# Kernel tuning notes

Measured on AMD Instinct MI355X. Metric: run time of the kernel, lower is better.

The kernel has to match this reference:

```python
import jax, jax.numpy as jnp
import numpy as np

B, S, D, H = 2, 2048, 1024, 16
HD = D // H  # head_dim = 64

def setup_inputs() -> dict:
    key = jax.random.key(0)
    ks = jax.random.split(key, 5)
    scale = 1.0 / np.sqrt(D)
    x = jax.random.normal(ks[0], (B, S, D), dtype=jnp.float32)
    Wq = jax.random.normal(ks[1], (D, D), dtype=jnp.float32) * scale
    Wk = jax.random.normal(ks[2], (D, D), dtype=jnp.float32) * scale
    Wv = jax.random.normal(ks[3], (D, D), dtype=jnp.float32) * scale
    Wf = jax.random.normal(ks[4], (D, D), dtype=jnp.float32) * scale
    z = jnp.zeros((D,), dtype=jnp.float32)
    return {"x": x, "Wq": Wq, "bq": z, "Wk": Wk, "bk": z, "Wv": Wv, "bv": z, "Wf": Wf, "bf": z}

def reference(x, Wq, bq, Wk, bk, Wv, bv, Wf, bf):
    # Linear layers follow torch convention: y = x @ W.T + b
    def split_heads(t):  # [B,S,D] -> [B,H,S,HD]
        return t.reshape(B, S, H, HD).transpose(0, 2, 1, 3)
    q = split_heads(x @ Wq.T + bq)
    k = split_heads(x @ Wk.T + bk)
    v = split_heads(x @ Wv.T + bv)
    scores = jnp.einsum('bhqd,bhkd->bhqk', q, k) / jnp.sqrt(jnp.float32(HD))
    causal = jnp.tril(jnp.ones((S, S), dtype=bool))  # [S,S]
    scores = jnp.where(causal[None, None], scores, -jnp.inf)
    attn = jax.nn.softmax(scores, axis=-1)
    out = jnp.einsum('bhqk,bhkd->bhqd', attn, v)
    out = out.transpose(0, 2, 1, 3).reshape(B, S, D)
    return out @ Wf.T + bf
```

## Files before the change

### kernel.cpp

```cpp
#include <hip/hip_runtime.h>
#include <stdint.h>

#define B_  2
#define S_  2048
#define D_  1024
#define H_  16
#define HD_ 64
#define M_  (B_*S_)

typedef __bf16 bf16x8 __attribute__((ext_vector_type(8)));
typedef float  f32x4  __attribute__((ext_vector_type(4)));
typedef unsigned short u16x8 __attribute__((ext_vector_type(8)));

typedef const __attribute__((address_space(1))) void* gas_ptr;
typedef __attribute__((address_space(3))) void* las_ptr;

__device__ __forceinline__ uint16_t f32_to_bf16(float f) {
  uint32_t u = __float_as_uint(f);
  u += 0x7FFFu + ((u >> 16) & 1u);
  return (uint16_t)(u >> 16);
}

__device__ __forceinline__ uint16_t f32_to_bf16_rtz(float f) {
  return (uint16_t)(__float_as_uint(f) >> 16);
}

__device__ __forceinline__ void g2l16(const uint16_t* g, uint16_t* l) {
  __builtin_amdgcn_global_load_lds((gas_ptr)g, (las_ptr)l, 16, 0, 0);
}

#define POFF(rt, kt, h) ((size_t)((((rt) * 16 + (kt)) * 2 + (h)) * 4096))

__global__ void cast_pack(const float* __restrict__ x,
                          const float* __restrict__ wq, const float* __restrict__ wk,
                          const float* __restrict__ wv, const float* __restrict__ wf,
                          uint16_t* __restrict__ xb,
                          uint16_t* __restrict__ wqb, uint16_t* __restrict__ wkb,
                          uint16_t* __restrict__ wvb, uint16_t* __restrict__ wfb) {
  const int XC = M_ * D_ / 8;
  const int WC = D_ * D_ / 8;
  int i = blockIdx.x * 256 + threadIdx.x;
  const float* src; uint16_t* dst; int off;
  if (i < XC) { src = x; dst = xb; off = i; }
  else {
    int j = i - XC;
    int w = j >> 17;
    off = j & (WC - 1);
    src = (w == 0) ? wq : (w == 1) ? wk : (w == 2) ? wv : wf;
    dst = (w == 0) ? wqb : (w == 1) ? wkb : (w == 2) ? wvb : wfb;
  }
  const int row = off >> 7;
  const int c   = off & 127;
  const float4 v0 = ((const float4*)src)[row * 256 + c * 2];
  const float4 v1 = ((const float4*)src)[row * 256 + c * 2 + 1];
  u16x8 o;
  o[0] = f32_to_bf16(v0.x); o[1] = f32_to_bf16(v0.y);
  o[2] = f32_to_bf16(v0.z); o[3] = f32_to_bf16(v0.w);
  o[4] = f32_to_bf16(v1.x); o[5] = f32_to_bf16(v1.y);
  o[6] = f32_to_bf16(v1.z); o[7] = f32_to_bf16(v1.w);
  const int kt = c >> 3, c8 = c & 7, h = c8 >> 2, c4 = c8 & 3;
  const int rt = row >> 7, r = row & 127;
  const int s = 4 * r + (c4 ^ ((r >> 1) & 3));
  *(u16x8*)(dst + POFF(rt, kt, h) + s * 8) = o;
}

__global__ __launch_bounds__(256, 2)
void qkv_gemm(const uint16_t* __restrict__ xb,
              const uint16_t* __restrict__ wqb, const uint16_t* __restrict__ wkb,
              const uint16_t* __restrict__ wvb,
              const float* __restrict__ bqv, const float* __restrict__ bkv,
              const float* __restrict__ bvv,
              uint16_t* __restrict__ qout, uint16_t* __restrict__ kout,
              uint16_t* __restrict__ vtout)
{
  __shared__ __align__(16) uint16_t As[2][2][4096];
  __shared__ __align__(16) uint16_t Bs[2][2][4096];

  const int wsel = blockIdx.x >> 3;
  const int nsel = blockIdx.x & 7;
  const int mtile = blockIdx.y;
  const int tid  = threadIdx.x;
  const int lane = tid & 63, wave = tid >> 6;
  const int quad = lane >> 4, l16 = lane & 15;
  const int wm = (wave >> 1) * 64, wn = (wave & 1) * 64;
  const int sw = quad ^ ((l16 >> 1) & 3);

  const uint16_t *Ap, *Bp;
  int art, brt, m0e, n0e;
  if (wsel < 2) {
    Ap = xb; art = mtile; Bp = (wsel == 0) ? wqb : wkb; brt = nsel;
    m0e = mtile * 128; n0e = nsel * 128;
  } else {
    Ap = wvb; art = nsel; Bp = xb; brt = mtile;
    m0e = nsel * 128; n0e = mtile * 128;
  }

  const int se0 = tid * 8;
  const int se1 = (256 + tid) * 8;
  const int ld0 = (wave * 64) * 8;
  const int ld1 = (256 + wave * 64) * 8;

  f32x4 acc[4][4];
  #pragma unroll
  for (int i = 0; i < 4; ++i)
    #pragma unroll
    for (int j = 0; j < 4; ++j)
      #pragma unroll
      for (int e = 0; e < 4; ++e)
        acc[i][j][e] = 0.f;

  #pragma unroll
  for (int h = 0; h < 2; ++h) {
    g2l16(Ap + POFF(art, 0, h) + se0, &As[0][h][ld0]);
    g2l16(Ap + POFF(art, 0, h) + se1, &As[0][h][ld1]);
    g2l16(Bp + POFF(brt, 0, h) + se0, &Bs[0][h][ld0]);
    g2l16(Bp + POFF(brt, 0, h) + se1, &Bs[0][h][ld1]);
  }
  __syncthreads();

  for (int t = 0; t < 16; ++t) {
    const int cb = t & 1, cn = cb ^ 1;
    if (t < 15) {
      #pragma unroll
      for (int h = 0; h < 2; ++h) {
        g2l16(Ap + POFF(art, t + 1, h) + se0, &As[cn][h][ld0]);
        g2l16(Ap + POFF(art, t + 1, h) + se1, &As[cn][h][ld1]);
        g2l16(Bp + POFF(brt, t + 1, h) + se0, &Bs[cn][h][ld0]);
        g2l16(Bp + POFF(brt, t + 1, h) + se1, &Bs[cn][h][ld1]);
      }
    }
    bf16x8 af[4][2], bf[4][2];
    #pragma unroll
    for (int mt = 0; mt < 4; ++mt) {
      const int ro = ((wm + mt * 16 + l16) * 4 + sw) * 8;
      af[mt][0] = *(const bf16x8*)(&As[cb][0][ro]);
      af[mt][1] = *(const bf16x8*)(&As[cb][1][ro]);
    }
    #pragma unroll
    for (int nt = 0; nt < 4; ++nt) {
      const int ro = ((wn + nt * 16 + l16) * 4 + sw) * 8;
      bf[nt][0] = *(const bf16x8*)(&Bs[cb][0][ro]);
      bf[nt][1] = *(const bf16x8*)(&Bs[cb][1][ro]);
    }
    __builtin_amdgcn_s_setprio(1);
    #pragma unroll
    for (int mt = 0; mt < 4; ++mt)
      #pragma unroll
      for (int nt = 0; nt < 4; ++nt) {
        acc[mt][nt] = __builtin_amdgcn_mfma_f32_16x16x32_bf16(
            af[mt][0], bf[nt][0], acc[mt][nt], 0, 0, 0);
        acc[mt][nt] = __builtin_amdgcn_mfma_f32_16x16x32_bf16(
            af[mt][1], bf[nt][1], acc[mt][nt], 0, 0, 0);
      }
    __builtin_amdgcn_s_setprio(0);
    __syncthreads();
  }

  if (wsel < 2) {
    const float* bias = (wsel == 0) ? bqv : bkv;
    uint16_t* outp = (wsel == 0) ? qout : kout;
    const float scl = (wsel == 0) ? 0.18033688f : 1.0f;
    #pragma unroll
    for (int nt = 0; nt < 4; ++nt) {
      const int n = n0e + wn + nt * 16 + l16;
      const int h = n >> 6, hd = n & 63;
      const float bia = bias[n];
      #pragma unroll
      for (int mt = 0; mt < 4; ++mt) {
        #pragma unroll
        for (int r = 0; r < 4; ++r) {
          const int m = m0e + wm + mt * 16 + quad * 4 + r;
          const int bb = m >> 11, s = m & (S_ - 1);
          outp[(((size_t)(bb * H_ + h)) * S_ + s) * HD_ + hd] =
              f32_to_bf16((acc[mt][nt][r] + bia) * scl);
        }
      }
    }
  } else {
    #pragma unroll
    for (int mt = 0; mt < 4; ++mt) {
      #pragma unroll
      for (int r = 0; r < 4; ++r) {
        const int m = m0e + wm + mt * 16 + quad * 4 + r;
        const int h = m >> 6, hd = m & 63;
        const float bia = bvv[m];
        #pragma unroll
        for (int nt = 0; nt < 4; ++nt) {
          const int n = n0e + wn + nt * 16 + l16;
          const int bb = n >> 11, s = n & (S_ - 1);
          vtout[(((size_t)(bb * H_ + h)) * HD_ + hd) * S_ + s] =
              f32_to_bf16(acc[mt][nt][r] + bia);
        }
      }
    }
  }
}

__global__ __launch_bounds__(256)
void flash_attn(const uint16_t* __restrict__ qb, const uint16_t* __restrict__ kb,
                const uint16_t* __restrict__ vtb, uint16_t* __restrict__ ao)
{
  __shared__ __align__(16) uint16_t ks[2][2][2048];
  __shared__ __align__(16) uint16_t vs[2][2][2048];
  __shared__ __align__(16) uint16_t p_lds[4][16][72];

  const int bh = blockIdx.x;
  const int qt = (int)(gridDim.y - 1u - blockIdx.y);
  const int wave = threadIdx.x >> 6, lane = threadIdx.x & 63;
  const int quad = lane >> 4, l16 = lane & 15;
  const int sw = quad ^ ((l16 >> 1) & 3);
  const int q0 = qt * 64;

  const uint16_t* Q  = qb  + (size_t)bh * S_ * HD_;
  const uint16_t* Kp = kb  + (size_t)bh * S_ * HD_;
  const uint16_t* Vt = vtb + (size_t)bh * HD_ * S_;

  const int qrow = q0 + wave * 16;
  bf16x8 aq0 = *(const bf16x8*)(Q + (size_t)(qrow + l16) * HD_ + quad * 8);
  bf16x8 aq1 = *(const bf16x8*)(Q + (size_t)(qrow + l16) * HD_ + 32 + quad * 8);

  const int srow = lane >> 2;
  const int schk = (lane & 3) ^ ((lane >> 3) & 3);
  const uint16_t* sb[4]; uint16_t* sd0[4]; uint16_t* sd1[4]; int sstep[4];
  #pragma unroll
  for (int j = 0; j < 4; ++j) {
    const int g = wave * 4 + j;
    if (g < 8) {
      const int c = (g >> 2) & 1, rb = g & 3;
      sd0[j] = &ks[0][c][rb * 512];
      sd1[j] = &ks[1][c][rb * 512];
      sb[j] = Kp + (size_t)(rb * 16 + srow) * HD_ + c * 32 + schk * 8;
      sstep[j] = 64 * HD_;
    } else {
      const int gg = g - 8, c = (gg >> 2) & 1, rb = gg & 3;
      sd0[j] = &vs[0][c][rb * 512];
      sd1[j] = &vs[1][c][rb * 512];
      sb[j] = Vt + (size_t)(rb * 16 + srow) * S_ + c * 32 + schk * 8;
      sstep[j] = 64;
    }
  }

  float lpart[4];
  f32x4 o[4];
  #pragma unroll
  for (int r = 0; r < 4; ++r) lpart[r] = 0.f;
  #pragma unroll
  for (int t = 0; t < 4; ++t)
    #pragma unroll
    for (int e = 0; e < 4; ++e) o[t][e] = 0.f;

  const int rowid = qrow + quad * 4;

  #pragma unroll
  for (int j = 0; j < 4; ++j) {
    g2l16(sb[j], sd0[j]);
    sb[j] += sstep[j];
  }
  __syncthreads();

  for (int kt = 0; kt <= qt; ++kt) {
    const int kbase = kt * 64;
    const bool diag = (kt == qt);
    const int cb = kt & 1;

    if (kt < qt) {
      #pragma unroll
      for (int j = 0; j < 4; ++j) {
        g2l16(sb[j], cb ? sd0[j] : sd1[j]);
        sb[j] += sstep[j];
      }
    }

    bf16x8 kf0[4], kf1[4];
    #pragma unroll
    for (int nt = 0; nt < 4; ++nt) {
      kf0[nt] = *(const bf16x8*)(&ks[cb][0][((nt * 16 + l16) * 4 + sw) * 8]);
      kf1[nt] = *(const bf16x8*)(&ks[cb][1][((nt * 16 + l16) * 4 + sw) * 8]);
    }
    f32x4 sacc[4];
    __builtin_amdgcn_s_setprio(1);
    #pragma unroll
    for (int nt = 0; nt < 4; ++nt) {
      #pragma unroll
      for (int e = 0; e < 4; ++e) sacc[nt][e] = 0.f;
      sacc[nt] = __builtin_amdgcn_mfma_f32_16x16x32_bf16(aq0, kf0[nt], sacc[nt], 0, 0, 0);
      sacc[nt] = __builtin_amdgcn_mfma_f32_16x16x32_bf16(aq1, kf1[nt], sacc[nt], 0, 0, 0);
    }
    __builtin_amdgcn_s_setprio(0);

    bf16x8 vf0[4], vf1[4];
    #pragma unroll
    for (int t = 0; t < 4; ++t) {
      vf0[t] = *(const bf16x8*)(&vs[cb][0][((t * 16 + l16) * 4 + sw) * 8]);
      vf1[t] = *(const bf16x8*)(&vs[cb][1][((t * 16 + l16) * 4 + sw) * 8]);
    }

    #pragma unroll
    for (int nt = 0; nt < 4; ++nt) {
      const int kkc = kbase + nt * 16 + l16;
      #pragma unroll
      for (int r = 0; r < 4; ++r) {
        float p = __builtin_amdgcn_exp2f(sacc[nt][r]);
        if (diag && (kkc > rowid + r)) p = 0.f;
        lpart[r] += p;
        p_lds[wave][quad * 4 + r][nt * 16 + l16] = f32_to_bf16_rtz(p);
      }
    }

    bf16x8 ap0 = *(const bf16x8*)(&p_lds[wave][l16][quad * 8]);
    bf16x8 ap1 = *(const bf16x8*)(&p_lds[wave][l16][32 + quad * 8]);
    __builtin_amdgcn_s_setprio(1);
    #pragma unroll
    for (int t = 0; t < 4; ++t) {
      o[t] = __builtin_amdgcn_mfma_f32_16x16x32_bf16(ap0, vf0[t], o[t], 0, 0, 0);
      o[t] = __builtin_amdgcn_mfma_f32_16x16x32_bf16(ap1, vf1[t], o[t], 0, 0, 0);
    }
    __builtin_amdgcn_s_setprio(0);
    __syncthreads();
  }

  #pragma unroll
  for (int r = 0; r < 4; ++r) {
    lpart[r] += __shfl_xor(lpart[r], 1, 64);
    lpart[r] += __shfl_xor(lpart[r], 2, 64);
    lpart[r] += __shfl_xor(lpart[r], 4, 64);
    lpart[r] += __shfl_xor(lpart[r], 8, 64);
  }
  const int bb = bh >> 4, h = bh & 15;
  #pragma unroll
  for (int t = 0; t < 4; ++t) {
    const int c8 = t * 2 + (l16 >> 3);
    const int hh = c8 >> 2, c4 = c8 & 3, e = l16 & 7;
    #pragma unroll
    for (int r = 0; r < 4; ++r) {
      const float ov = o[t][r] / lpart[r];
      const int grow = bb * S_ + rowid + r;
      const int rt = grow >> 7, rr = grow & 127;
      const int s = 4 * rr + (c4 ^ ((rr >> 1) & 3));
      ao[POFF(rt, h, hh) + s * 8 + e] = f32_to_bf16(ov);
    }
  }
}

__global__ __launch_bounds__(256, 2)
void out_gemm(const uint16_t* __restrict__ ab, const uint16_t* __restrict__ wfb,
              const float* __restrict__ bfv, float* __restrict__ out)
{
  __shared__ __align__(16) uint16_t As[2][2][4096];
  __shared__ __align__(16) uint16_t Bs[2][2][4096];
  const int nsel = blockIdx.x;
  const int mtile = blockIdx.y;
  const int tid  = threadIdx.x;
  const int lane = tid & 63, wave = tid >> 6;
  const int quad = lane >> 4, l16 = lane & 15;
  const int wm = (wave >> 1) * 64, wn = (wave & 1) * 64;
  const int sw = quad ^ ((l16 >> 1) & 3);

  const int se0 = tid * 8, se1 = (256 + tid) * 8;
  const int ld0 = (wave * 64) * 8, ld1 = (256 + wave * 64) * 8;

  f32x4 acc[4][4];
  #pragma unroll
  for (int i = 0; i < 4; ++i)
    #pragma unroll
    for (int j = 0; j < 4; ++j)
      #pragma unroll
      for (int e = 0; e < 4; ++e)
        acc[i][j][e] = 0.f;

  #pragma unroll
  for (int h = 0; h < 2; ++h) {
    g2l16(ab  + POFF(mtile, 0, h) + se0, &As[0][h][ld0]);
    g2l16(ab  + POFF(mtile, 0, h) + se1, &As[0][h][ld1]);
    g2l16(wfb + POFF(nsel, 0, h) + se0, &Bs[0][h][ld0]);
    g2l16(wfb + POFF(nsel, 0, h) + se1, &Bs[0][h][ld1]);
  }
  __syncthreads();

  for (int t = 0; t < 16; ++t) {
    const int cb = t & 1, cn = cb ^ 1;
    if (t < 15) {
      #pragma unroll
      for (int h = 0; h < 2; ++h) {
        g2l16(ab  + POFF(mtile, t + 1, h) + se0, &As[cn][h][ld0]);
        g2l16(ab  + POFF(mtile, t + 1, h) + se1, &As[cn][h][ld1]);
        g2l16(wfb + POFF(nsel, t + 1, h) + se0, &Bs[cn][h][ld0]);
        g2l16(wfb + POFF(nsel, t + 1, h) + se1, &Bs[cn][h][ld1]);
      }
    }
    bf16x8 af[4][2], bf[4][2];
    #pragma unroll
    for (int mt = 0; mt < 4; ++mt) {
      const int ro = ((wm + mt * 16 + l16) * 4 + sw) * 8;
      af[mt][0] = *(const bf16x8*)(&As[cb][0][ro]);
      af[mt][1] = *(const bf16x8*)(&As[cb][1][ro]);
    }
    #pragma unroll
    for (int nt = 0; nt < 4; ++nt) {
      const int ro = ((wn + nt * 16 + l16) * 4 + sw) * 8;
      bf[nt][0] = *(const bf16x8*)(&Bs[cb][0][ro]);
      bf[nt][1] = *(const bf16x8*)(&Bs[cb][1][ro]);
    }
    __builtin_amdgcn_s_setprio(1);
    #pragma unroll
    for (int mt = 0; mt < 4; ++mt)
      #pragma unroll
      for (int nt = 0; nt < 4; ++nt) {
        acc[mt][nt] = __builtin_amdgcn_mfma_f32_16x16x32_bf16(
            af[mt][0], bf[nt][0], acc[mt][nt], 0, 0, 0);
        acc[mt][nt] = __builtin_amdgcn_mfma_f32_16x16x32_bf16(
            af[mt][1], bf[nt][1], acc[mt][nt], 0, 0, 0);
      }
    __builtin_amdgcn_s_setprio(0);
    __syncthreads();
  }

  const int m0 = mtile * 128, n0 = nsel * 128;
  #pragma unroll
  for (int nt = 0; nt < 4; ++nt) {
    const int n = n0 + wn + nt * 16 + l16;
    const float bia = bfv[n];
    #pragma unroll
    for (int mt = 0; mt < 4; ++mt) {
      #pragma unroll
      for (int r = 0; r < 4; ++r) {
        const int m = m0 + wm + mt * 16 + quad * 4 + r;
        out[(size_t)m * D_ + n] = acc[mt][nt][r] + bia;
      }
    }
  }
}

extern "C" void kernel_launch(void* const* d_in, const int* in_sizes, int n_in,
                              void* d_out, int out_size, void* d_ws, size_t ws_size,
                              hipStream_t stream) {
  (void)in_sizes; (void)n_in; (void)out_size; (void)ws_size;
  const float* x  = (const float*)d_in[0];
  const float* Wq = (const float*)d_in[1];
  const float* bq = (const float*)d_in[2];
  const float* Wk = (const float*)d_in[3];
  const float* bk = (const float*)d_in[4];
  const float* Wv = (const float*)d_in[5];
  const float* bv = (const float*)d_in[6];
  const float* Wf = (const float*)d_in[7];
  const float* bf = (const float*)d_in[8];
  float* out = (float*)d_out;

  uint16_t* ws = (uint16_t*)d_ws;
  uint16_t* xb   = ws;
  uint16_t* wqb  = xb  + (size_t)M_ * D_;
  uint16_t* wkb  = wqb + (size_t)D_ * D_;
  uint16_t* wvb  = wkb + (size_t)D_ * D_;
  uint16_t* wfb  = wvb + (size_t)D_ * D_;
  uint16_t* qbuf = wfb + (size_t)D_ * D_;
  uint16_t* kbuf = qbuf + (size_t)M_ * D_;
  uint16_t* vtb  = kbuf + (size_t)M_ * D_;
  uint16_t* aob  = vtb  + (size_t)M_ * D_;

  const int CAST_BLOCKS = (M_ * D_ / 8 + 4 * (D_ * D_ / 8)) / 256;
  cast_pack<<<CAST_BLOCKS, 256, 0, stream>>>(x, Wq, Wk, Wv, Wf,
                                             xb, wqb, wkb, wvb, wfb);

  qkv_gemm<<<dim3(24, 32), 256, 0, stream>>>(xb, wqb, wkb, wvb, bq, bk, bv,
                                             qbuf, kbuf, vtb);
  flash_attn<<<dim3(32, 32), 256, 0, stream>>>(qbuf, kbuf, vtb, aob);
  out_gemm<<<dim3(8, 32), 256, 0, stream>>>(aob, wfb, bf, out);
}
```

Baseline: 182.3 us.

## Enlarge QKV GEMM block tile to 256x128 with single-half K steps

Each qkv_gemm block now computes a 256x128 output tile instead of 128x128. Each wave covers 128 rows with 8x4 MFMA accumulators. The K loop is split into 32 half-width steps so that shared memory stays small while the A tile doubles. The V-path block index is remapped to fit the halved grid. The aim is more reuse of each B tile and less global/LDS traffic per FLOP. The costs are higher register pressure, twice as many barriers, and only 384 blocks, which may fill the CUs unevenly.

```diff
diff --git a/kernel.cpp b/kernel.cpp
--- a/kernel.cpp
+++ b/kernel.cpp
@@ -74,7 +74,7 @@
               uint16_t* __restrict__ vtout)
 {
   __shared__ __align__(16) uint16_t As[2][2][4096];
-  __shared__ __align__(16) uint16_t Bs[2][2][4096];
+  __shared__ __align__(16) uint16_t Bs[2][4096];
 
   const int wsel = blockIdx.x >> 3;
   const int nsel = blockIdx.x & 7;
@@ -82,17 +82,23 @@
   const int tid  = threadIdx.x;
   const int lane = tid & 63, wave = tid >> 6;
   const int quad = lane >> 4, l16 = lane & 15;
-  const int wm = (wave >> 1) * 64, wn = (wave & 1) * 64;
+  const int wm = (wave >> 1) * 128;
+  const int wn = (wave & 1) * 64;
+  const int rh = wave >> 1;
   const int sw = quad ^ ((l16 >> 1) & 3);
 
   const uint16_t *Ap, *Bp;
   int art, brt, m0e, n0e;
   if (wsel < 2) {
-    Ap = xb; art = mtile; Bp = (wsel == 0) ? wqb : wkb; brt = nsel;
-    m0e = mtile * 128; n0e = nsel * 128;
+    Ap = xb; art = mtile * 2;
+    Bp = (wsel == 0) ? wqb : wkb; brt = nsel;
+    m0e = mtile * 256; n0e = nsel * 128;
   } else {
-    Ap = wvb; art = nsel; Bp = xb; brt = mtile;
-    m0e = nsel * 128; n0e = mtile * 128;
+    const int idv = nsel + 8 * mtile;
+    const int artv = idv >> 5;
+    const int brtv = idv & 31;
+    Ap = wvb; art = artv * 2; Bp = xb; brt = brtv;
+    m0e = artv * 256; n0e = brtv * 128;
   }
 
   const int se0 = tid * 8;
@@ -100,58 +106,48 @@
   const int ld0 = (wave * 64) * 8;
   const int ld1 = (256 + wave * 64) * 8;
 
-  f32x4 acc[4][4];
-  #pragma unroll
-  for (int i = 0; i < 4; ++i)
+  f32x4 acc[8][4];
+  #pragma unroll
+  for (int i = 0; i < 8; ++i)
     #pragma unroll
     for (int j = 0; j < 4; ++j)
       #pragma unroll
       for (int e = 0; e < 4; ++e)
         acc[i][j][e] = 0.f;
 
-  #pragma unroll
-  for (int h = 0; h < 2; ++h) {
-    g2l16(Ap + POFF(art, 0, h) + se0, &As[0][h][ld0]);
-    g2l16(Ap + POFF(art, 0, h) + se1, &As[0][h][ld1]);
-    g2l16(Bp + POFF(brt, 0, h) + se0, &Bs[0][h][ld0]);
-    g2l16(Bp + POFF(brt, 0, h) + se1, &Bs[0][h][ld1]);
-  }
+  g2l16(Ap + POFF(art,     0, 0) + se0, &As[0][0][ld0]);
+  g2l16(Ap + POFF(art,     0, 0) + se1, &As[0][0][ld1]);
+  g2l16(Ap + POFF(art + 1, 0, 0) + se0, &As[0][1][ld0]);
+  g2l16(Ap + POFF(art + 1, 0, 0) + se1, &As[0][1][ld1]);
+  g2l16(Bp + POFF(brt,     0, 0) + se0, &Bs[0][ld0]);
+  g2l16(Bp + POFF(brt,     0, 0) + se1, &Bs[0][ld1]);
   __syncthreads();
 
-  for (int t = 0; t < 16; ++t) {
+  for (int t = 0; t < 32; ++t) {
     const int cb = t & 1, cn = cb ^ 1;
-    if (t < 15) {
-      #pragma unroll
-      for (int h = 0; h < 2; ++h) {
-        g2l16(Ap + POFF(art, t + 1, h) + se0, &As[cn][h][ld0]);
-        g2l16(Ap + POFF(art, t + 1, h) + se1, &As[cn][h][ld1]);
-        g2l16(Bp + POFF(brt, t + 1, h) + se0, &Bs[cn][h][ld0]);
-        g2l16(Bp + POFF(brt, t + 1, h) + se1, &Bs[cn][h][ld1]);
-      }
-    }
-    bf16x8 af[4][2], bf[4][2];
-    #pragma unroll
-    for (int mt = 0; mt < 4; ++mt) {
-      const int ro = ((wm + mt * 16 + l16) * 4 + sw) * 8;
-      af[mt][0] = *(const bf16x8*)(&As[cb][0][ro]);
-      af[mt][1] = *(const bf16x8*)(&As[cb][1][ro]);
-    }
-    #pragma unroll
-    for (int nt = 0; nt < 4; ++nt) {
-      const int ro = ((wn + nt * 16 + l16) * 4 + sw) * 8;
-      bf[nt][0] = *(const bf16x8*)(&Bs[cb][0][ro]);
-      bf[nt][1] = *(const bf16x8*)(&Bs[cb][1][ro]);
-    }
+    if (t < 31) {
+      const int kt = (t + 1) >> 1, h = (t + 1) & 1;
+      g2l16(Ap + POFF(art,     kt, h) + se0, &As[cn][0][ld0]);
+      g2l16(Ap + POFF(art,     kt, h) + se1, &As[cn][0][ld1]);
+      g2l16(Ap + POFF(art + 1, kt, h) + se0, &As[cn][1][ld0]);
+      g2l16(Ap + POFF(art + 1, kt, h) + se1, &As[cn][1][ld1]);
+      g2l16(Bp + POFF(brt,     kt, h) + se0, &Bs[cn][ld0]);
+      g2l16(Bp + POFF(brt,     kt, h) + se1, &Bs[cn][ld1]);
+    }
+    bf16x8 af[8], bf[4];
+    #pragma unroll
+    for (int mt = 0; mt < 8; ++mt)
+      af[mt] = *(const bf16x8*)(&As[cb][rh][((mt * 16 + l16) * 4 + sw) * 8]);
+    #pragma unroll
+    for (int nt = 0; nt < 4; ++nt)
+      bf[nt] = *(const bf16x8*)(&Bs[cb][((wn + nt * 16 + l16) * 4 + sw) * 8]);
     __builtin_amdgcn_s_setprio(1);
     #pragma unroll
-    for (int mt = 0; mt < 4; ++mt)
-      #pragma unroll
-      for (int nt = 0; nt < 4; ++nt) {
+    for (int mt = 0; mt < 8; ++mt)
+      #pragma unroll
+      for (int nt = 0; nt < 4; ++nt)
         acc[mt][nt] = __builtin_amdgcn_mfma_f32_16x16x32_bf16(
-            af[mt][0], bf[nt][0], acc[mt][nt], 0, 0, 0);
-        acc[mt][nt] = __builtin_amdgcn_mfma_f32_16x16x32_bf16(
-            af[mt][1], bf[nt][1], acc[mt][nt], 0, 0, 0);
-      }
+            af[mt], bf[nt], acc[mt][nt], 0, 0, 0);
     __builtin_amdgcn_s_setprio(0);
     __syncthreads();
   }
@@ -166,7 +162,7 @@
       const int h = n >> 6, hd = n & 63;
       const float bia = bias[n];
       #pragma unroll
-      for (int mt = 0; mt < 4; ++mt) {
+      for (int mt = 0; mt < 8; ++mt) {
         #pragma unroll
         for (int r = 0; r < 4; ++r) {
           const int m = m0e + wm + mt * 16 + quad * 4 + r;
@@ -178,7 +174,7 @@
     }
   } else {
     #pragma unroll
-    for (int mt = 0; mt < 4; ++mt) {
+    for (int mt = 0; mt < 8; ++mt) {
       #pragma unroll
       for (int r = 0; r < 4; ++r) {
         const int m = m0e + wm + mt * 16 + quad * 4 + r;
@@ -461,7 +457,7 @@
   cast_pack<<<CAST_BLOCKS, 256, 0, stream>>>(x, Wq, Wk, Wv, Wf,
                                              xb, wqb, wkb, wvb, wfb);
 
-  qkv_gemm<<<dim3(24, 32), 256, 0, stream>>>(xb, wqb, wkb, wvb, bq, bk, bv,
+  qkv_gemm<<<dim3(24, 16), 256, 0, stream>>>(xb, wqb, wkb, wvb, bq, bk, bv,
                                              qbuf, kbuf, vtb);
   flash_attn<<<dim3(32, 32), 256, 0, stream>>>(qbuf, kbuf, vtb, aob);
   out_gemm<<<dim3(8, 32), 256, 0, stream>>>(aob, wfb, bf, out);
```

Result: no change. 180.5 us (-1.0%).
